# Optimization experiments

Measured on AMD Instinct MI355X. Metric: run time of the kernel, lower is better.

## Reference

```python
import jax, jax.numpy as jnp
import numpy as np

N_NODES = 50000
N_EDGES = 1_600_000
D_IN, D_HID, D_OUT = 128, 512, 64


def _graph_conv(h, src, dst, W_rel, b_rel, W_root, n_nodes):
    # PyG GraphConv with aggr='add':
    #   out_i = W_rel @ (sum_{j->i} h_j) + b_rel + W_root @ h_i
    agg = jax.ops.segment_sum(h[src], dst, num_segments=n_nodes)  # [N, d]
    return agg @ W_rel + b_rel + h @ W_root


def setup_inputs() -> dict:
    key = jax.random.key(0)
    ks = jax.random.split(key, 12)
    def glorot(k, shape):
        fan_in, fan_out = shape
        lim = (6.0 / (fan_in + fan_out)) ** 0.5
        return jax.random.uniform(k, shape, jnp.float32, -lim, lim)
    x = jax.random.normal(ks[0], (N_NODES, D_IN), jnp.float32)
    edge_index = jax.random.randint(ks[1], (2, N_EDGES), 0, N_NODES, jnp.int64)
    return {
        "x": x,
        "W1_rel": glorot(ks[2], (D_IN, D_HID)),
        "b1": jnp.zeros((D_HID,), jnp.float32),
        "W1_root": glorot(ks[3], (D_IN, D_HID)),
        "W2_rel": glorot(ks[4], (D_HID, D_HID)),
        "b2": jnp.zeros((D_HID,), jnp.float32),
        "W2_root": glorot(ks[5], (D_HID, D_HID)),
        "W3_rel": glorot(ks[6], (D_HID, D_HID)),
        "b3": jnp.zeros((D_HID,), jnp.float32),
        "W3_root": glorot(ks[7], (D_HID, D_HID)),
        "W_lin": glorot(ks[8], (D_HID, D_OUT)),
        "b_lin": jnp.zeros((D_OUT,), jnp.float32),
        "edge_index": edge_index,
    }


def reference(x, W1_rel, b1, W1_root, W2_rel, b2, W2_root,
              W3_rel, b3, W3_root, W_lin, b_lin, edge_index):
    n = x.shape[0]
    src, dst = edge_index[0], edge_index[1]
    h = jax.nn.relu(_graph_conv(x, src, dst, W1_rel, b1, W1_root, n))
    h = jax.nn.relu(_graph_conv(h, src, dst, W2_rel, b2, W2_root, n))
    h = jax.nn.relu(_graph_conv(h, src, dst, W3_rel, b3, W3_root, n))
    node_embed = h
    # dropout is identity in eval mode; final linear head
    logits = h @ W_lin + b_lin
    return (logits, node_embed)
```

## Files before the change

### kernel.cpp

```cpp
#include <hip/hip_runtime.h>


typedef unsigned short u16;
typedef unsigned int u32;
typedef unsigned char u8;

#define NN 50000
#define NE 1600000
#define MPAD 50176
#define GRID_M ((NN + 127) / 128)
#define NBKT 98
#define CAP 20480
#define STG 18432

using frag8 = __attribute__((ext_vector_type(8))) short;
using f32x4 = __attribute__((ext_vector_type(4))) float;
using f32x2 = __attribute__((ext_vector_type(2))) float;

__device__ __forceinline__ u16 f2bf(float f) {
  u32 u = __float_as_uint(f);
  u32 r = u + 0x7fffu + ((u >> 16) & 1u);
  return (u16)(r >> 16);
}
__device__ __forceinline__ float lo2f(u32 u) { return __uint_as_float(u << 16); }
__device__ __forceinline__ float hi2f(u32 u) { return __uint_as_float(u & 0xffff0000u); }
__device__ __forceinline__ u32 pack2(float a, float b) {
  return (u32)f2bf(a) | ((u32)f2bf(b) << 16);
}

__device__ __forceinline__ void g2l16(const void* g, void* l) {
  __builtin_amdgcn_global_load_lds((const __attribute__((address_space(1))) void*)g,
                                   (__attribute__((address_space(3))) void*)l, 16, 0, 0);
}


__global__ void zero_i32(int* p, int n) {
  int i = blockIdx.x * 256 + threadIdx.x;
  if (i < n) p[i] = 0;
}

__global__ __launch_bounds__(256) void p1bin(const int* __restrict__ src,
                                             const int* __restrict__ dst,
                                             int* __restrict__ gcur,
                                             u32* __restrict__ region, int ne) {
  __shared__ u32 lbuf[NBKT * 64];
  __shared__ int lcnt[NBKT];
  __shared__ int gbase[NBKT];
  const int tid = threadIdx.x;
  if (tid < NBKT) lcnt[tid] = 0;
  __syncthreads();
  const int base = blockIdx.x * 2048;
#pragma unroll
  for (int j = 0; j < 8; ++j) {
    int i = base + j * 256 + tid;
    if (i < ne) {
      int d = dst[i];
      int s = src[i];
      int b = d >> 9;
      u32 entry = ((u32)(d & 511) << 16) | (u32)s;
      int slot = atomicAdd(&lcnt[b], 1);
      if (slot < 64) lbuf[b * 64 + slot] = entry;
      else {
        int g = atomicAdd(&gcur[b], 1);
        region[(size_t)b * CAP + g] = entry;
      }
    }
  }
  __syncthreads();
  if (tid < NBKT) {
    int c = min(lcnt[tid], 64);
    gbase[tid] = atomicAdd(&gcur[tid], c);
  }
  __syncthreads();
  const int wv = tid >> 6, lane = tid & 63;
  for (int b = wv; b < NBKT; b += 4) {
    int c = min(lcnt[b], 64);
    int gb = gbase[b];
    for (int s2 = lane; s2 < c; s2 += 64)
      region[(size_t)b * CAP + gb + s2] = lbuf[b * 64 + s2];
  }
}

__global__ void scan98(const int* __restrict__ gcur, int* __restrict__ bbase,
                       int* __restrict__ rs) {
  if (threadIdx.x == 0) {
    int run = 0;
    for (int b = 0; b < NBKT; ++b) {
      bbase[b] = run;
      run += gcur[b];
    }
    bbase[NBKT] = run;
    rs[NN] = run;
  }
}

__global__ __launch_bounds__(256) void p2build(const u32* __restrict__ region,
                                               const int* __restrict__ gcnt,
                                               const int* __restrict__ bbase,
                                               int* __restrict__ rs,
                                               u16* __restrict__ csr) {
  __shared__ int cnt[512];
  __shared__ int off[512];
  __shared__ int sh[256];
  __shared__ u16 stg[STG];
  const int b = blockIdx.x, tid = threadIdx.x;
  const int n0 = b * 512;
  const int nnb = min(512, NN - n0);
  const int ec = gcnt[b];
  const int gb = bbase[b];
  const u32* __restrict__ reg = region + (size_t)b * CAP;
  cnt[tid] = 0;
  cnt[tid + 256] = 0;
  __syncthreads();
  for (int i = tid; i < ec; i += 256) atomicAdd(&cnt[reg[i] >> 16], 1);
  __syncthreads();
  int c0 = cnt[2 * tid], c1 = cnt[2 * tid + 1];
  int s = c0 + c1;
  sh[tid] = s;
  __syncthreads();
  for (int o = 1; o < 256; o <<= 1) {
    int t2 = (tid >= o) ? sh[tid - o] : 0;
    __syncthreads();
    sh[tid] += t2;
    __syncthreads();
  }
  int base0 = sh[tid] - s;
  off[2 * tid] = base0;
  off[2 * tid + 1] = base0 + c0;
  __syncthreads();
  if (2 * tid < nnb) rs[n0 + 2 * tid] = gb + off[2 * tid];
  if (2 * tid + 1 < nnb) rs[n0 + 2 * tid + 1] = gb + off[2 * tid + 1];
  cnt[2 * tid] = off[2 * tid];
  cnt[2 * tid + 1] = off[2 * tid + 1];
  __syncthreads();
  for (int i = tid; i < ec; i += 256) {
    u32 e = reg[i];
    int slot = atomicAdd(&cnt[e >> 16], 1);
    u16 sv = (u16)(e & 0xffff);
    if (slot < STG) stg[slot] = sv;
    else csr[gb + slot] = sv;
  }
  __syncthreads();
  for (int i = tid; i < ec && i < STG; i += 256) csr[gb + i] = stg[i];
}


__global__ void f2bf_x(const float4* __restrict__ in, u16* __restrict__ out, int n4) {
  int i = blockIdx.x * 256 + threadIdx.x;
  if (i < n4) {
    float4 v = in[i];
    int node = i >> 5;
    int w = i & 31;
    uint2 o;
    o.x = pack2(v.x, v.y);
    o.y = pack2(v.z, v.w);
    *(uint2*)(out + (size_t)node * 256 + 128 + w * 4) = o;
  }
}

__global__ void wtrans(const float* __restrict__ Wa, int Ka, const float* __restrict__ Wb,
                       int Kb, int N, u16* __restrict__ out) {
  int idx = blockIdx.x * 256 + threadIdx.x;
  int Kt = Ka + Kb;
  if (idx >= N * Kt) return;
  int n = idx / Kt;
  int k = idx - n * Kt;
  float v = (k < Ka) ? Wa[(size_t)k * N + n] : Wb[(size_t)(k - Ka) * N + n];
  out[idx] = f2bf(v);
}


__device__ __forceinline__ void accb(f32x2* a, uint4 v, float s) {
  f32x2 sv = (f32x2){s, s};
  f32x2 f;
  f.x = lo2f(v.x); f.y = hi2f(v.x); a[0] += f * sv;
  f.x = lo2f(v.y); f.y = hi2f(v.y); a[1] += f * sv;
  f.x = lo2f(v.z); f.y = hi2f(v.z); a[2] += f * sv;
  f.x = lo2f(v.w); f.y = hi2f(v.w); a[3] += f * sv;
}

__global__ __launch_bounds__(256) void agg_bf128(const u16* __restrict__ H, int ldh,
                                                 u16* __restrict__ Out, int ldo,
                                                 const int* __restrict__ rs,
                                                 const u16* __restrict__ csr, int n) {
  int w = (blockIdx.x * 256 + threadIdx.x) >> 6;
  int lane = threadIdx.x & 63;
  if (w >= n) return;
  int beg = rs[w], end = rs[w + 1];
  const int q = lane >> 4;
  const int lsub = lane & 15;
  f32x2 acc[4];
#pragma unroll
  for (int i = 0; i < 4; ++i) acc[i] = (f32x2){0.f, 0.f};

  int e = beg;
  for (; e + 16 <= end; e += 16) {
    int si[4];
#pragma unroll
    for (int u = 0; u < 4; ++u) si[u] = csr[e + 4 * u + q];
    uint4 v[4];
#pragma unroll
    for (int u = 0; u < 4; ++u)
      v[u] = *(const uint4*)(H + (size_t)si[u] * ldh + lsub * 8);
#pragma unroll
    for (int u = 0; u < 4; ++u) accb(acc, v[u], 1.f);
  }
  if (e < end) {
#pragma unroll
    for (int u = 0; u < 4; ++u) {
      int ei = e + 4 * u + q;
      int ec = min(ei, end - 1);
      int s0 = csr[ec];
      uint4 v = *(const uint4*)(H + (size_t)s0 * ldh + lsub * 8);
      accb(acc, v, (ei < end) ? 1.f : 0.f);
    }
  }
#pragma unroll
  for (int i = 0; i < 4; ++i) {
    acc[i].x += __shfl_xor(acc[i].x, 16);
    acc[i].y += __shfl_xor(acc[i].y, 16);
    acc[i].x += __shfl_xor(acc[i].x, 32);
    acc[i].y += __shfl_xor(acc[i].y, 32);
  }
  if (lane < 32) {
    int qq = lane >> 4;
    uint2 o;
    o.x = pack2(acc[qq * 2].x, acc[qq * 2].y);
    o.y = pack2(acc[qq * 2 + 1].x, acc[qq * 2 + 1].y);
    *(uint2*)(Out + (size_t)w * ldo + (lane & 15) * 8 + qq * 4) = o;
  }
}


__device__ __forceinline__ void accp(f32x2* a, uint4 v, float s) {
  f32x2 sv = (f32x2){s, s};
  f32x2 f;
  f = __builtin_amdgcn_cvt_pk_f32_fp8(v.x, false); a[0] += f * sv;
  f = __builtin_amdgcn_cvt_pk_f32_fp8(v.x, true);  a[1] += f * sv;
  f = __builtin_amdgcn_cvt_pk_f32_fp8(v.y, false); a[2] += f * sv;
  f = __builtin_amdgcn_cvt_pk_f32_fp8(v.y, true);  a[3] += f * sv;
  f = __builtin_amdgcn_cvt_pk_f32_fp8(v.z, false); a[4] += f * sv;
  f = __builtin_amdgcn_cvt_pk_f32_fp8(v.z, true);  a[5] += f * sv;
  f = __builtin_amdgcn_cvt_pk_f32_fp8(v.w, false); a[6] += f * sv;
  f = __builtin_amdgcn_cvt_pk_f32_fp8(v.w, true);  a[7] += f * sv;
}

__global__ __launch_bounds__(256) void agg_fp8(const u8* __restrict__ H8,
                                               const float* __restrict__ sc,
                                               u16* __restrict__ Out,
                                               const int* __restrict__ rs,
                                               const u16* __restrict__ csr, int n) {
  int w = (blockIdx.x * 256 + threadIdx.x) >> 6;
  int lane = threadIdx.x & 63;
  if (w >= n) return;
  int beg = rs[w], end = rs[w + 1];
  const int halfe = lane >> 5;
  const int lsub = lane & 31;
  const int shalf = lsub >> 4;
  f32x2 acc[8];
#pragma unroll
  for (int i = 0; i < 8; ++i) acc[i] = (f32x2){0.f, 0.f};

  int e = beg;
  for (; e + 8 <= end; e += 8) {
    int si[4];
#pragma unroll
    for (int u = 0; u < 4; ++u) si[u] = csr[e + 2 * u + halfe];
    uint4 v[4];
#pragma unroll
    for (int u = 0; u < 4; ++u)
      v[u] = *(const uint4*)(H8 + (size_t)si[u] * 512 + lsub * 16);
    float cs[4];
#pragma unroll
    for (int u = 0; u < 4; ++u) cs[u] = sc[si[u] * 2 + shalf];
#pragma unroll
    for (int u = 0; u < 4; ++u) accp(acc, v[u], cs[u]);
  }
  if (e < end) {
#pragma unroll
    for (int u = 0; u < 4; ++u) {
      int ei = e + 2 * u + halfe;
      int ec = min(ei, end - 1);
      int s0 = csr[ec];
      uint4 v = *(const uint4*)(H8 + (size_t)s0 * 512 + lsub * 16);
      float c = (ei < end) ? sc[s0 * 2 + shalf] : 0.f;
      accp(acc, v, c);
    }
  }
#pragma unroll
  for (int i = 0; i < 8; ++i) {
    acc[i].x += __shfl_xor(acc[i].x, 32);
    acc[i].y += __shfl_xor(acc[i].y, 32);
  }
  uint4 o;
  if (halfe == 0) {
    o.x = pack2(acc[0].x, acc[0].y);
    o.y = pack2(acc[1].x, acc[1].y);
    o.z = pack2(acc[2].x, acc[2].y);
    o.w = pack2(acc[3].x, acc[3].y);
  } else {
    o.x = pack2(acc[4].x, acc[4].y);
    o.y = pack2(acc[5].x, acc[5].y);
    o.z = pack2(acc[6].x, acc[6].y);
    o.w = pack2(acc[7].x, acc[7].y);
  }
  *(uint4*)(Out + (size_t)w * 512 + lsub * 16 + halfe * 8) = o;
}


__global__ __launch_bounds__(512, 4) void gemm256(
    const u16* __restrict__ A1, int lda1, const u16* __restrict__ A2, int lda2, int K1,
    int Ktot, const u16* __restrict__ Bt, const float* __restrict__ bias, int relu,
    u16* __restrict__ out_bf, int ldob, float* __restrict__ out_f32, int ldof,
    u8* __restrict__ out_fp8, float* __restrict__ out_sc, int M) {
  __shared__ u16 lA[128 * 32];
  __shared__ u16 lB[256 * 32];
  __shared__ u32 smaxu[128];
  const int tid = threadIdx.x;
  const int lane = tid & 63;
  const int wv = tid >> 6;
  const int wm = (wv >> 2) * 64;
  const int wn = (wv & 3) * 64;
  const int n0 = blockIdx.x * 256;
  const int m0 = blockIdx.y * 128;
  const int r15 = lane & 15;
  const int quad = lane >> 4;

  if (tid < 128) smaxu[tid] = 0;

  f32x4 acc[4][4];
#pragma unroll
  for (int i = 0; i < 4; ++i)
#pragma unroll
    for (int j = 0; j < 4; ++j) acc[i][j] = (f32x4){0.f, 0.f, 0.f, 0.f};

  for (int kk = 0; kk < Ktot; kk += 32) {
    const u16* Ab;
    int lda;
    if (kk < K1) { Ab = A1 + kk; lda = lda1; }
    else         { Ab = A2 + (kk - K1); lda = lda2; }
    {
      int row = tid >> 2;
      int kc = (tid & 3) * 8;
      g2l16(Ab + (size_t)(m0 + row) * lda + kc, &lA[tid * 8]);
    }
#pragma unroll
    for (int i = 0; i < 2; ++i) {
      int li = tid + i * 512;
      int nrow = li >> 2;
      int kc = (li & 3) * 8;
      g2l16(Bt + (size_t)(n0 + nrow) * Ktot + (kk + kc), &lB[li * 8]);
    }
    __syncthreads();
    frag8 af[4], bfr[4];
#pragma unroll
    for (int mt = 0; mt < 4; ++mt)
      af[mt] = *(const frag8*)&lA[(wm + mt * 16 + r15) * 32 + quad * 8];
#pragma unroll
    for (int nt = 0; nt < 4; ++nt)
      bfr[nt] = *(const frag8*)&lB[(wn + nt * 16 + r15) * 32 + quad * 8];
#pragma unroll
    for (int mt = 0; mt < 4; ++mt)
#pragma unroll
      for (int nt = 0; nt < 4; ++nt)
        acc[mt][nt] =
            __builtin_amdgcn_mfma_f32_16x16x32_bf16(af[mt], bfr[nt], acc[mt][nt], 0, 0, 0);
    __syncthreads();
  }

#pragma unroll
  for (int mt = 0; mt < 4; ++mt) {
#pragma unroll
    for (int r = 0; r < 4; ++r) {
      float rm = 0.f;
#pragma unroll
      for (int nt = 0; nt < 4; ++nt) {
        int c = n0 + wn + nt * 16 + r15;
        float v = acc[mt][nt][r] + bias[c];
        if (relu) v = fmaxf(v, 0.f);
        acc[mt][nt][r] = v;
        rm = fmaxf(rm, v);
      }
      if (out_fp8) {
        rm = fmaxf(rm, __shfl_xor(rm, 1));
        rm = fmaxf(rm, __shfl_xor(rm, 2));
        rm = fmaxf(rm, __shfl_xor(rm, 4));
        rm = fmaxf(rm, __shfl_xor(rm, 8));
        if (r15 == 0) atomicMax(&smaxu[wm + mt * 16 + quad * 4 + r], __float_as_uint(rm));
      }
    }
  }
  if (out_fp8) __syncthreads();

#pragma unroll
  for (int mt = 0; mt < 4; ++mt) {
    int rloc = wm + mt * 16 + quad * 4;
#pragma unroll
    for (int r = 0; r < 4; ++r) {
      int row = m0 + rloc + r;
      if (row < M) {
        float inv = 0.f;
        if (out_fp8) {
          float s = __uint_as_float(smaxu[rloc + r]);
          inv = (s > 0.f) ? 448.f / s : 0.f;
          if (r15 == 0 && wn == 0)
            out_sc[row * 2 + (n0 >> 8)] = (s > 0.f) ? s / 448.f : 0.f;
        }
#pragma unroll
        for (int nt = 0; nt < 4; ++nt) {
          int c = n0 + wn + nt * 16 + r15;
          float v = acc[mt][nt][r];
          if (out_f32) out_f32[(size_t)row * ldof + c] = v;
          if (out_bf) out_bf[(size_t)row * ldob + c] = f2bf(v);
        }
        if (out_fp8) {
          u32 u01 = (u32)__builtin_amdgcn_cvt_pk_fp8_f32(acc[mt][0][r] * inv,
                                                         acc[mt][1][r] * inv, 0, false);
          u32 u23 = (u32)__builtin_amdgcn_cvt_pk_fp8_f32(acc[mt][2][r] * inv,
                                                         acc[mt][3][r] * inv, 0, false);
          size_t rb = (size_t)row * 512 + n0 + wn + r15;
          out_fp8[rb] = (u8)(u01 & 0xff);
          out_fp8[rb + 16] = (u8)((u01 >> 8) & 0xff);
          out_fp8[rb + 32] = (u8)(u23 & 0xff);
          out_fp8[rb + 48] = (u8)((u23 >> 8) & 0xff);
        }
      }
    }
  }
}


__global__ __launch_bounds__(256) void gemm64(
    const u16* __restrict__ A1, int lda1, int Ktot, const u16* __restrict__ Bt,
    const float* __restrict__ bias, float* __restrict__ out_f32, int ldof, int M) {
  __shared__ u16 lA[128 * 32];
  __shared__ u16 lB[64 * 32];
  const int tid = threadIdx.x;
  const int lane = tid & 63;
  const int wv = tid >> 6;
  const int wm = (wv >> 1) * 64;
  const int wn = (wv & 1) * 32;
  const int m0 = blockIdx.x * 128;
  const int r15 = lane & 15;
  const int quad = lane >> 4;

  f32x4 acc[4][2];
#pragma unroll
  for (int i = 0; i < 4; ++i)
#pragma unroll
    for (int j = 0; j < 2; ++j) acc[i][j] = (f32x4){0.f, 0.f, 0.f, 0.f};

  for (int kk = 0; kk < Ktot; kk += 32) {
#pragma unroll
    for (int i = 0; i < 2; ++i) {
      int li = tid + i * 256;
      int row = li >> 2;
      int kc = (li & 3) * 8;
      g2l16(A1 + (size_t)(m0 + row) * lda1 + kk + kc, &lA[li * 8]);
    }
    {
      int nrow = tid >> 2;
      int kc = (tid & 3) * 8;
      if (tid < 256) g2l16(Bt + (size_t)nrow * Ktot + (kk + kc), &lB[tid * 8]);
    }
    __syncthreads();
    frag8 af[4], bfr[2];
#pragma unroll
    for (int mt = 0; mt < 4; ++mt)
      af[mt] = *(const frag8*)&lA[(wm + mt * 16 + r15) * 32 + quad * 8];
#pragma unroll
    for (int nt = 0; nt < 2; ++nt)
      bfr[nt] = *(const frag8*)&lB[(wn + nt * 16 + r15) * 32 + quad * 8];
#pragma unroll
    for (int mt = 0; mt < 4; ++mt)
#pragma unroll
      for (int nt = 0; nt < 2; ++nt)
        acc[mt][nt] =
            __builtin_amdgcn_mfma_f32_16x16x32_bf16(af[mt], bfr[nt], acc[mt][nt], 0, 0, 0);
    __syncthreads();
  }

#pragma unroll
  for (int mt = 0; mt < 4; ++mt) {
    int rbase = m0 + wm + mt * 16 + quad * 4;
#pragma unroll
    for (int r = 0; r < 4; ++r) {
      int row = rbase + r;
      if (row < M) {
#pragma unroll
        for (int nt = 0; nt < 2; ++nt) {
          int c = wn + nt * 16 + r15;
          out_f32[(size_t)row * ldof + c] = acc[mt][nt][r] + bias[c];
        }
      }
    }
  }
}


extern "C" void kernel_launch(void* const* d_in, const int* in_sizes, int n_in, void* d_out,
                              int out_size, void* d_ws, size_t ws_size, hipStream_t stream) {
  const float* x = (const float*)d_in[0];
  const float* W1r = (const float*)d_in[1];
  const float* b1 = (const float*)d_in[2];
  const float* W1o = (const float*)d_in[3];
  const float* W2r = (const float*)d_in[4];
  const float* b2 = (const float*)d_in[5];
  const float* W2o = (const float*)d_in[6];
  const float* W3r = (const float*)d_in[7];
  const float* b3 = (const float*)d_in[8];
  const float* W3o = (const float*)d_in[9];
  const float* Wl = (const float*)d_in[10];
  const float* bl = (const float*)d_in[11];
  const int* src = (const int*)d_in[12];
  const int* dst = src + NE;

  size_t off = 0;
  char* ws = (char*)d_ws;
  auto take = [&](size_t bytes) -> void* {
    void* p = ws + off;
    off = (off + bytes + 255) & ~(size_t)255;
    return p;
  };
  u16* h13 = (u16*)take((size_t)MPAD * 512 * 2);
  u16* h2 = (u16*)take((size_t)MPAD * 512 * 2);
  u16* aggB = (u16*)take((size_t)MPAD * 512 * 2);
  u16* aggx = aggB;
  u8* hfp8 = (u8*)take((size_t)MPAD * 512);
  float* scb = (float*)take((size_t)MPAD * 2 * 4);
  u16* wt1 = (u16*)take((size_t)512 * 256 * 2);
  u16* wt2 = (u16*)take((size_t)512 * 1024 * 2);
  u16* wt3 = (u16*)take((size_t)512 * 1024 * 2);
  u16* wtl = (u16*)take((size_t)64 * 512 * 2);
  u32* region = (u32*)take((size_t)NBKT * CAP * 4);
  int* gcur = (int*)take(128 * 4);
  int* bbase = (int*)take(128 * 4);
  int* rs = (int*)take((size_t)(NN + 1) * 4);
  u16* csr = (u16*)take((size_t)NE * 2);

  float* out_logits = (float*)d_out;
  float* out_embed = out_logits + (size_t)NN * 64;

  zero_i32<<<1, 128, 0, stream>>>(gcur, NBKT);
  p1bin<<<(NE + 2047) / 2048, 256, 0, stream>>>(src, dst, gcur, region, NE);
  scan98<<<1, 64, 0, stream>>>(gcur, bbase, rs);
  p2build<<<NBKT, 256, 0, stream>>>(region, gcur, bbase, rs, csr);

  f2bf_x<<<(NN * 32 + 255) / 256, 256, 0, stream>>>((const float4*)x, aggx, NN * 32);
  wtrans<<<(512 * 256 + 255) / 256, 256, 0, stream>>>(W1r, 128, W1o, 128, 512, wt1);
  wtrans<<<(512 * 1024 + 255) / 256, 256, 0, stream>>>(W2r, 512, W2o, 512, 512, wt2);
  wtrans<<<(512 * 1024 + 255) / 256, 256, 0, stream>>>(W3r, 512, W3o, 512, 512, wt3);
  wtrans<<<(64 * 512 + 255) / 256, 256, 0, stream>>>(Wl, 512, Wl, 0, 64, wtl);

  agg_bf128<<<(NN + 3) / 4, 256, 0, stream>>>(aggx + 128, 256, aggx, 256, rs, csr, NN);
  gemm256<<<dim3(2, GRID_M), 512, 0, stream>>>(aggx, 256, aggx, 256, 256, 256, wt1, b1, 1,
                                               h13, 512, (float*)nullptr, 0, hfp8, scb, NN);
  agg_fp8<<<(NN + 3) / 4, 256, 0, stream>>>(hfp8, scb, aggB, rs, csr, NN);
  gemm256<<<dim3(2, GRID_M), 512, 0, stream>>>(aggB, 512, h13, 512, 512, 1024, wt2, b2, 1,
                                               h2, 512, (float*)nullptr, 0, hfp8, scb, NN);
  agg_fp8<<<(NN + 3) / 4, 256, 0, stream>>>(hfp8, scb, aggB, rs, csr, NN);
  gemm256<<<dim3(2, GRID_M), 512, 0, stream>>>(aggB, 512, h2, 512, 512, 1024, wt3, b3, 1,
                                               h13, 512, out_embed, 512, (u8*)nullptr,
                                               (float*)nullptr, NN);
  gemm64<<<GRID_M, 256, 0, stream>>>(h13, 512, 512, wtl, bl, out_logits, 64, NN);
}
```

Measured before the change: 746.3 us.

## Slice feature tables into column passes so gather working set fits cache

After: 1.177 ms. +57.6%, slower.

```diff
diff --git a/kernel.cpp b/kernel.cpp
--- a/kernel.cpp
+++ b/kernel.cpp
@@ -16,6 +16,7 @@
 using frag8 = __attribute__((ext_vector_type(8))) short;
 using f32x4 = __attribute__((ext_vector_type(4))) float;
 using f32x2 = __attribute__((ext_vector_type(2))) float;
+using u32x4 = __attribute__((ext_vector_type(4))) unsigned int;
 
 __device__ __forceinline__ u16 f2bf(float f) {
   u32 u = __float_as_uint(f);
@@ -145,7 +146,8 @@
 }
 
 
-__global__ void f2bf_x(const float4* __restrict__ in, u16* __restrict__ out, int n4) {
+__global__ void f2bf_x(const float4* __restrict__ in, u16* __restrict__ out,
+                       u16* __restrict__ xsl, int n4) {
   int i = blockIdx.x * 256 + threadIdx.x;
   if (i < n4) {
     float4 v = in[i];
@@ -155,6 +157,7 @@
     o.x = pack2(v.x, v.y);
     o.y = pack2(v.z, v.w);
     *(uint2*)(out + (size_t)node * 256 + 128 + w * 4) = o;
+    *(uint2*)(xsl + ((size_t)(w >> 3) * MPAD + node) * 32 + (w & 7) * 4) = o;
   }
 }
 
@@ -178,59 +181,6 @@
   f.x = lo2f(v.z); f.y = hi2f(v.z); a[2] += f * sv;
   f.x = lo2f(v.w); f.y = hi2f(v.w); a[3] += f * sv;
 }
-
-__global__ __launch_bounds__(256) void agg_bf128(const u16* __restrict__ H, int ldh,
-                                                 u16* __restrict__ Out, int ldo,
-                                                 const int* __restrict__ rs,
-                                                 const u16* __restrict__ csr, int n) {
-  int w = (blockIdx.x * 256 + threadIdx.x) >> 6;
-  int lane = threadIdx.x & 63;
-  if (w >= n) return;
-  int beg = rs[w], end = rs[w + 1];
-  const int q = lane >> 4;
-  const int lsub = lane & 15;
-  f32x2 acc[4];
-#pragma unroll
-  for (int i = 0; i < 4; ++i) acc[i] = (f32x2){0.f, 0.f};
-
-  int e = beg;
-  for (; e + 16 <= end; e += 16) {
-    int si[4];
-#pragma unroll
-    for (int u = 0; u < 4; ++u) si[u] = csr[e + 4 * u + q];
-    uint4 v[4];
-#pragma unroll
-    for (int u = 0; u < 4; ++u)
-      v[u] = *(const uint4*)(H + (size_t)si[u] * ldh + lsub * 8);
-#pragma unroll
-    for (int u = 0; u < 4; ++u) accb(acc, v[u], 1.f);
-  }
-  if (e < end) {
-#pragma unroll
-    for (int u = 0; u < 4; ++u) {
-      int ei = e + 4 * u + q;
-      int ec = min(ei, end - 1);
-      int s0 = csr[ec];
-      uint4 v = *(const uint4*)(H + (size_t)s0 * ldh + lsub * 8);
-      accb(acc, v, (ei < end) ? 1.f : 0.f);
-    }
-  }
-#pragma unroll
-  for (int i = 0; i < 4; ++i) {
-    acc[i].x += __shfl_xor(acc[i].x, 16);
-    acc[i].y += __shfl_xor(acc[i].y, 16);
-    acc[i].x += __shfl_xor(acc[i].x, 32);
-    acc[i].y += __shfl_xor(acc[i].y, 32);
-  }
-  if (lane < 32) {
-    int qq = lane >> 4;
-    uint2 o;
-    o.x = pack2(acc[qq * 2].x, acc[qq * 2].y);
-    o.y = pack2(acc[qq * 2 + 1].x, acc[qq * 2 + 1].y);
-    *(uint2*)(Out + (size_t)w * ldo + (lane & 15) * 8 + qq * 4) = o;
-  }
-}
-
 
 __device__ __forceinline__ void accp(f32x2* a, uint4 v, float s) {
   f32x2 sv = (f32x2){s, s};
@@ -245,66 +195,94 @@
   f = __builtin_amdgcn_cvt_pk_f32_fp8(v.w, true);  a[7] += f * sv;
 }
 
-__global__ __launch_bounds__(256) void agg_fp8(const u8* __restrict__ H8,
-                                               const float* __restrict__ sc,
-                                               u16* __restrict__ Out,
-                                               const int* __restrict__ rs,
-                                               const u16* __restrict__ csr, int n) {
+__global__ __launch_bounds__(256) void agg_bf128s(const u16* __restrict__ Hs,
+                                                  u16* __restrict__ Out,
+                                                  const int* __restrict__ rs,
+                                                  const u16* __restrict__ csr, int n,
+                                                  int pass) {
   int w = (blockIdx.x * 256 + threadIdx.x) >> 6;
   int lane = threadIdx.x & 63;
   if (w >= n) return;
   int beg = rs[w], end = rs[w + 1];
-  const int halfe = lane >> 5;
-  const int lsub = lane & 31;
-  const int shalf = lsub >> 4;
-  f32x2 acc[8];
-#pragma unroll
-  for (int i = 0; i < 8; ++i) acc[i] = (f32x2){0.f, 0.f};
-
-  int e = beg;
-  for (; e + 8 <= end; e += 8) {
-    int si[4];
-#pragma unroll
-    for (int u = 0; u < 4; ++u) si[u] = csr[e + 2 * u + halfe];
-    uint4 v[4];
-#pragma unroll
-    for (int u = 0; u < 4; ++u)
-      v[u] = *(const uint4*)(H8 + (size_t)si[u] * 512 + lsub * 16);
-    float cs[4];
-#pragma unroll
-    for (int u = 0; u < 4; ++u) cs[u] = sc[si[u] * 2 + shalf];
-#pragma unroll
-    for (int u = 0; u < 4; ++u) accp(acc, v[u], cs[u]);
-  }
-  if (e < end) {
-#pragma unroll
-    for (int u = 0; u < 4; ++u) {
-      int ei = e + 2 * u + halfe;
-      int ec = min(ei, end - 1);
-      int s0 = csr[ec];
-      uint4 v = *(const uint4*)(H8 + (size_t)s0 * 512 + lsub * 16);
-      float c = (ei < end) ? sc[s0 * 2 + shalf] : 0.f;
-      accp(acc, v, c);
-    }
-  }
-#pragma unroll
-  for (int i = 0; i < 8; ++i) {
-    acc[i].x += __shfl_xor(acc[i].x, 32);
-    acc[i].y += __shfl_xor(acc[i].y, 32);
-  }
-  uint4 o;
-  if (halfe == 0) {
+  const int eg = lane >> 2;
+  const int ls = lane & 3;
+  const u16* __restrict__ Hp = Hs + (size_t)pass * MPAD * 32;
+  f32x2 acc[4];
+#pragma unroll
+  for (int i = 0; i < 4; ++i) acc[i] = (f32x2){0.f, 0.f};
+  for (int e = beg; e < end; e += 32) {
+#pragma unroll
+    for (int u = 0; u < 2; ++u) {
+      int ei = e + u * 16 + eg;
+      if (ei < end) {
+        int si = csr[ei];
+        uint4 v = *(const uint4*)(Hp + (size_t)si * 32 + ls * 8);
+        accb(acc, v, 1.f);
+      }
+    }
+  }
+#pragma unroll
+  for (int i = 0; i < 4; ++i) {
+    acc[i].x += __shfl_xor(acc[i].x, 4);  acc[i].y += __shfl_xor(acc[i].y, 4);
+    acc[i].x += __shfl_xor(acc[i].x, 8);  acc[i].y += __shfl_xor(acc[i].y, 8);
+    acc[i].x += __shfl_xor(acc[i].x, 16); acc[i].y += __shfl_xor(acc[i].y, 16);
+    acc[i].x += __shfl_xor(acc[i].x, 32); acc[i].y += __shfl_xor(acc[i].y, 32);
+  }
+  if (eg == 0) {
+    u32x4 o;
     o.x = pack2(acc[0].x, acc[0].y);
     o.y = pack2(acc[1].x, acc[1].y);
     o.z = pack2(acc[2].x, acc[2].y);
     o.w = pack2(acc[3].x, acc[3].y);
-  } else {
-    o.x = pack2(acc[4].x, acc[4].y);
-    o.y = pack2(acc[5].x, acc[5].y);
-    o.z = pack2(acc[6].x, acc[6].y);
-    o.w = pack2(acc[7].x, acc[7].y);
-  }
-  *(uint4*)(Out + (size_t)w * 512 + lsub * 16 + halfe * 8) = o;
+    __builtin_nontemporal_store(o, (u32x4*)(Out + (size_t)w * 256 + pass * 32 + ls * 8));
+  }
+}
+
+__global__ __launch_bounds__(256) void agg_fp8s(const u8* __restrict__ H8,
+                                                const float* __restrict__ sc,
+                                                u16* __restrict__ Out,
+                                                const int* __restrict__ rs,
+                                                const u16* __restrict__ csr, int n,
+                                                int pass) {
+  int w = (blockIdx.x * 256 + threadIdx.x) >> 6;
+  int lane = threadIdx.x & 63;
+  if (w >= n) return;
+  int beg = rs[w], end = rs[w + 1];
+  const int eg = lane >> 2;
+  const int ls = lane & 3;
+  const int shalf = pass >> 2;
+  const u8* __restrict__ Hp = H8 + (size_t)pass * MPAD * 64;
+  f32x2 acc[8];
+#pragma unroll
+  for (int i = 0; i < 8; ++i) acc[i] = (f32x2){0.f, 0.f};
+  for (int e = beg; e < end; e += 32) {
+#pragma unroll
+    for (int u = 0; u < 2; ++u) {
+      int ei = e + u * 16 + eg;
+      if (ei < end) {
+        int si = csr[ei];
+        uint4 v = *(const uint4*)(Hp + (size_t)si * 64 + ls * 16);
+        accp(acc, v, sc[si * 2 + shalf]);
+      }
+    }
+  }
+#pragma unroll
+  for (int i = 0; i < 8; ++i) {
+    acc[i].x += __shfl_xor(acc[i].x, 4);  acc[i].y += __shfl_xor(acc[i].y, 4);
+    acc[i].x += __shfl_xor(acc[i].x, 8);  acc[i].y += __shfl_xor(acc[i].y, 8);
+    acc[i].x += __shfl_xor(acc[i].x, 16); acc[i].y += __shfl_xor(acc[i].y, 16);
+    acc[i].x += __shfl_xor(acc[i].x, 32); acc[i].y += __shfl_xor(acc[i].y, 32);
+  }
+  if (eg == 0) {
+    u32x4 o1, o2;
+    o1.x = pack2(acc[0].x, acc[0].y); o1.y = pack2(acc[1].x, acc[1].y);
+    o1.z = pack2(acc[2].x, acc[2].y); o1.w = pack2(acc[3].x, acc[3].y);
+    o2.x = pack2(acc[4].x, acc[4].y); o2.y = pack2(acc[5].x, acc[5].y);
+    o2.z = pack2(acc[6].x, acc[6].y); o2.w = pack2(acc[7].x, acc[7].y);
+    u16* dp = Out + (size_t)w * 512 + pass * 64 + ls * 16;
+    __builtin_nontemporal_store(o1, (u32x4*)dp);
+    __builtin_nontemporal_store(o2, (u32x4*)(dp + 8));
+  }
 }
 
 
@@ -418,11 +396,12 @@
                                                          acc[mt][1][r] * inv, 0, false);
           u32 u23 = (u32)__builtin_amdgcn_cvt_pk_fp8_f32(acc[mt][2][r] * inv,
                                                          acc[mt][3][r] * inv, 0, false);
-          size_t rb = (size_t)row * 512 + n0 + wn + r15;
-          out_fp8[rb] = (u8)(u01 & 0xff);
-          out_fp8[rb + 16] = (u8)((u01 >> 8) & 0xff);
-          out_fp8[rb + 32] = (u8)(u23 & 0xff);
-          out_fp8[rb + 48] = (u8)((u23 >> 8) & 0xff);
+          int c0 = n0 + wn + r15;
+          u8* pb = out_fp8 + ((size_t)(c0 >> 6) * MPAD + row) * 64 + (c0 & 63);
+          pb[0] = (u8)(u01 & 0xff);
+          pb[16] = (u8)((u01 >> 8) & 0xff);
+          pb[32] = (u8)(u23 & 0xff);
+          pb[48] = (u8)((u23 >> 8) & 0xff);
         }
       }
     }
@@ -526,6 +505,7 @@
   u16* h2 = (u16*)take((size_t)MPAD * 512 * 2);
   u16* aggB = (u16*)take((size_t)MPAD * 512 * 2);
   u16* aggx = aggB;
+  u16* xsl = aggB + (size_t)MPAD * 256;
   u8* hfp8 = (u8*)take((size_t)MPAD * 512);
   float* scb = (float*)take((size_t)MPAD * 2 * 4);
   u16* wt1 = (u16*)take((size_t)512 * 256 * 2);
@@ -546,19 +526,22 @@
   scan98<<<1, 64, 0, stream>>>(gcur, bbase, rs);
   p2build<<<NBKT, 256, 0, stream>>>(region, gcur, bbase, rs, csr);
 
-  f2bf_x<<<(NN * 32 + 255) / 256, 256, 0, stream>>>((const float4*)x, aggx, NN * 32);
+  f2bf_x<<<(NN * 32 + 255) / 256, 256, 0, stream>>>((const float4*)x, aggx, xsl, NN * 32);
   wtrans<<<(512 * 256 + 255) / 256, 256, 0, stream>>>(W1r, 128, W1o, 128, 512, wt1);
   wtrans<<<(512 * 1024 + 255) / 256, 256, 0, stream>>>(W2r, 512, W2o, 512, 512, wt2);
   wtrans<<<(512 * 1024 + 255) / 256, 256, 0, stream>>>(W3r, 512, W3o, 512, 512, wt3);
   wtrans<<<(64 * 512 + 255) / 256, 256, 0, stream>>>(Wl, 512, Wl, 0, 64, wtl);
 
-  agg_bf128<<<(NN + 3) / 4, 256, 0, stream>>>(aggx + 128, 256, aggx, 256, rs, csr, NN);
+  for (int p = 0; p < 4; ++p)
+    agg_bf128s<<<(NN + 3) / 4, 256, 0, stream>>>(xsl, aggx, rs, csr, NN, p);
   gemm256<<<dim3(2, GRID_M), 512, 0, stream>>>(aggx, 256, aggx, 256, 256, 256, wt1, b1, 1,
                                                h13, 512, (float*)nullptr, 0, hfp8, scb, NN);
-  agg_fp8<<<(NN + 3) / 4, 256, 0, stream>>>(hfp8, scb, aggB, rs, csr, NN);
+  for (int p = 0; p < 8; ++p)
+    agg_fp8s<<<(NN + 3) / 4, 256, 0, stream>>>(hfp8, scb, aggB, rs, csr, NN, p);
   gemm256<<<dim3(2, GRID_M), 512, 0, stream>>>(aggB, 512, h13, 512, 512, 1024, wt2, b2, 1,
                                                h2, 512, (float*)nullptr, 0, hfp8, scb, NN);
-  agg_fp8<<<(NN + 3) / 4, 256, 0, stream>>>(hfp8, scb, aggB, rs, csr, NN);
+  for (int p = 0; p < 8; ++p)
+    agg_fp8s<<<(NN + 3) / 4, 256, 0, stream>>>(hfp8, scb, aggB, rs, csr, NN, p);
   gemm256<<<dim3(2, GRID_M), 512, 0, stream>>>(aggB, 512, h2, 512, 512, 1024, wt3, b3, 1,
                                                h13, 512, out_embed, 512, (u8*)nullptr,
                                                (float*)nullptr, NN);
```

## Double-buffer LDS tiles in gemm256 and gemm64 to overlap loads with MFMA

Applied to the files above, without the earlier changes.

Result: faster. 727.8 us (median of 2 runs) (-2.5%).

```diff
diff --git a/kernel.cpp b/kernel.cpp
--- a/kernel.cpp
+++ b/kernel.cpp
@@ -313,8 +313,8 @@
     int Ktot, const u16* __restrict__ Bt, const float* __restrict__ bias, int relu,
     u16* __restrict__ out_bf, int ldob, float* __restrict__ out_f32, int ldof,
     u8* __restrict__ out_fp8, float* __restrict__ out_sc, int M) {
-  __shared__ u16 lA[128 * 32];
-  __shared__ u16 lB[256 * 32];
+  __shared__ u16 lA[2][128 * 32];
+  __shared__ u16 lB[2][256 * 32];
   __shared__ u32 smaxu[128];
   const int tid = threadIdx.x;
   const int lane = tid & 63;
@@ -328,37 +328,41 @@
 
   if (tid < 128) smaxu[tid] = 0;
 
-  f32x4 acc[4][4];
-#pragma unroll
-  for (int i = 0; i < 4; ++i)
-#pragma unroll
-    for (int j = 0; j < 4; ++j) acc[i][j] = (f32x4){0.f, 0.f, 0.f, 0.f};
-
-  for (int kk = 0; kk < Ktot; kk += 32) {
+  const int arow = tid >> 2;
+  const int akc = (tid & 3) * 8;
+
+  auto stage = [&](int kk, int b) {
     const u16* Ab;
     int lda;
     if (kk < K1) { Ab = A1 + kk; lda = lda1; }
     else         { Ab = A2 + (kk - K1); lda = lda2; }
-    {
-      int row = tid >> 2;
-      int kc = (tid & 3) * 8;
-      g2l16(Ab + (size_t)(m0 + row) * lda + kc, &lA[tid * 8]);
-    }
+    g2l16(Ab + (size_t)(m0 + arow) * lda + akc, &lA[b][tid * 8]);
 #pragma unroll
     for (int i = 0; i < 2; ++i) {
       int li = tid + i * 512;
-      int nrow = li >> 2;
-      int kc = (li & 3) * 8;
-      g2l16(Bt + (size_t)(n0 + nrow) * Ktot + (kk + kc), &lB[li * 8]);
-    }
-    __syncthreads();
+      g2l16(Bt + (size_t)(n0 + (li >> 2)) * Ktot + (kk + (li & 3) * 8), &lB[b][li * 8]);
+    }
+  };
+
+  f32x4 acc[4][4];
+#pragma unroll
+  for (int i = 0; i < 4; ++i)
+#pragma unroll
+    for (int j = 0; j < 4; ++j) acc[i][j] = (f32x4){0.f, 0.f, 0.f, 0.f};
+
+  stage(0, 0);
+  __syncthreads();
+  const int ntk = Ktot >> 5;
+  for (int t = 0; t < ntk; ++t) {
+    const int cur = t & 1;
+    if (t + 1 < ntk) stage((t + 1) * 32, cur ^ 1);
     frag8 af[4], bfr[4];
 #pragma unroll
     for (int mt = 0; mt < 4; ++mt)
-      af[mt] = *(const frag8*)&lA[(wm + mt * 16 + r15) * 32 + quad * 8];
+      af[mt] = *(const frag8*)&lA[cur][(wm + mt * 16 + r15) * 32 + quad * 8];
 #pragma unroll
     for (int nt = 0; nt < 4; ++nt)
-      bfr[nt] = *(const frag8*)&lB[(wn + nt * 16 + r15) * 32 + quad * 8];
+      bfr[nt] = *(const frag8*)&lB[cur][(wn + nt * 16 + r15) * 32 + quad * 8];
 #pragma unroll
     for (int mt = 0; mt < 4; ++mt)
 #pragma unroll
@@ -433,8 +437,8 @@
 __global__ __launch_bounds__(256) void gemm64(
     const u16* __restrict__ A1, int lda1, int Ktot, const u16* __restrict__ Bt,
     const float* __restrict__ bias, float* __restrict__ out_f32, int ldof, int M) {
-  __shared__ u16 lA[128 * 32];
-  __shared__ u16 lB[64 * 32];
+  __shared__ u16 lA[2][128 * 32];
+  __shared__ u16 lB[2][64 * 32];
   const int tid = threadIdx.x;
   const int lane = tid & 63;
   const int wv = tid >> 6;
@@ -444,33 +448,34 @@
   const int r15 = lane & 15;
   const int quad = lane >> 4;
 
-  f32x4 acc[4][2];
-#pragma unroll
-  for (int i = 0; i < 4; ++i)
-#pragma unroll
-    for (int j = 0; j < 2; ++j) acc[i][j] = (f32x4){0.f, 0.f, 0.f, 0.f};
-
-  for (int kk = 0; kk < Ktot; kk += 32) {
+  auto stage = [&](int kk, int b) {
 #pragma unroll
     for (int i = 0; i < 2; ++i) {
       int li = tid + i * 256;
-      int row = li >> 2;
-      int kc = (li & 3) * 8;
-      g2l16(A1 + (size_t)(m0 + row) * lda1 + kk + kc, &lA[li * 8]);
-    }
-    {
-      int nrow = tid >> 2;
-      int kc = (tid & 3) * 8;
-      if (tid < 256) g2l16(Bt + (size_t)nrow * Ktot + (kk + kc), &lB[tid * 8]);
-    }
-    __syncthreads();
+      g2l16(A1 + (size_t)(m0 + (li >> 2)) * lda1 + kk + (li & 3) * 8, &lA[b][li * 8]);
+    }
+    g2l16(Bt + (size_t)(tid >> 2) * Ktot + (kk + (tid & 3) * 8), &lB[b][tid * 8]);
+  };
+
+  f32x4 acc[4][2];
+#pragma unroll
+  for (int i = 0; i < 4; ++i)
+#pragma unroll
+    for (int j = 0; j < 2; ++j) acc[i][j] = (f32x4){0.f, 0.f, 0.f, 0.f};
+
+  stage(0, 0);
+  __syncthreads();
+  const int ntk = Ktot >> 5;
+  for (int t = 0; t < ntk; ++t) {
+    const int cur = t & 1;
+    if (t + 1 < ntk) stage((t + 1) * 32, cur ^ 1);
     frag8 af[4], bfr[2];
 #pragma unroll
     for (int mt = 0; mt < 4; ++mt)
-      af[mt] = *(const frag8*)&lA[(wm + mt * 16 + r15) * 32 + quad * 8];
+      af[mt] = *(const frag8*)&lA[cur][(wm + mt * 16 + r15) * 32 + quad * 8];
 #pragma unroll
     for (int nt = 0; nt < 2; ++nt)
-      bfr[nt] = *(const frag8*)&lB[(wn + nt * 16 + r15) * 32 + quad * 8];
+      bfr[nt] = *(const frag8*)&lB[cur][(wn + nt * 16 + r15) * 32 + quad * 8];
 #pragma unroll
     for (int mt = 0; mt < 4; ++mt)
 #pragma unroll
```
